# Performance work log

Measured on AMD Instinct MI355X. Metric: run time of the kernel, lower is better.

The kernel has to match this reference:

```python
import jax, jax.numpy as jnp
import numpy as np


def _conv(x, w, pad):
    # NCHW conv, stride 1
    return jax.lax.conv_general_dilated(
        x, w, window_strides=(1, 1), padding=pad,
        dimension_numbers=("NCHW", "OIHW", "NCHW"))


def _deform_conv(x, off_w, off_b, w, b, kh, kw, ph, pw):
    """DCNv2-style modulated deformable conv, stride 1, zero padding."""
    B, C, H, W = x.shape
    K = kh * kw
    om = _conv(x, off_w, ((ph, ph), (pw, pw))) + off_b[None, :, None, None]  # [B,3K,H,W]
    dy, dx, m = om[:, :K], om[:, K:2 * K], om[:, 2 * K:]
    mask = jax.nn.sigmoid(m)  # [B,K,H,W]
    ky = (jnp.repeat(jnp.arange(kh), kw) - ph).astype(x.dtype)  # [K]
    kx = (jnp.tile(jnp.arange(kw), kh) - pw).astype(x.dtype)    # [K]
    hh = jnp.arange(H, dtype=x.dtype)[None, None, :, None]
    ww = jnp.arange(W, dtype=x.dtype)[None, None, None, :]
    py = dy + ky[None, :, None, None] + hh  # [B,K,H,W] sampling y
    px = dx + kx[None, :, None, None] + ww  # [B,K,H,W] sampling x
    y0 = jnp.floor(py)
    x0 = jnp.floor(px)
    ty = py - y0
    tx = px - x0
    y0i = y0.astype(jnp.int32)
    x0i = x0.astype(jnp.int32)
    bidx = jnp.arange(B)[:, None, None, None]

    def gather(yi, xi):
        valid = (yi >= 0) & (yi < H) & (xi >= 0) & (xi < W)
        yc = jnp.clip(yi, 0, H - 1)
        xc = jnp.clip(xi, 0, W - 1)
        v = x[bidx, :, yc, xc]  # [B,K,H,W,C]
        return v * valid[..., None].astype(x.dtype)

    val = (gather(y0i, x0i) * ((1 - ty) * (1 - tx))[..., None]
           + gather(y0i, x0i + 1) * ((1 - ty) * tx)[..., None]
           + gather(y0i + 1, x0i) * (ty * (1 - tx))[..., None]
           + gather(y0i + 1, x0i + 1) * (ty * tx)[..., None])
    val = val * mask[..., None]  # modulation
    out = jnp.einsum('bkhwc,ock->bohw', val, w.reshape(w.shape[0], C, K))
    return out + b[None, :, None, None]


def _preprocess(x, w1, b1, w2, b2):
    h = _conv(x, w1, ((0, 0), (0, 0))) + b1[None, :, None, None]
    return _conv(h, w2, ((0, 0), (0, 0))) + b2[None, :, None, None]


def setup_inputs() -> dict:
    key = jax.random.key(0)
    ks = jax.random.split(key, 12)
    B, C, H, W = 4, 64, 256, 256
    k = 3
    s = 0.05
    inp = {
        "a_low": jax.random.normal(ks[0], (B, C, H, W), jnp.float32),
        "a_high": jax.random.normal(ks[1], (B, C, H, W), jnp.float32),
        # preprocess: Conv 64->32 (1x1), Conv 32->64 (1x1)
        "pre_w1": jax.random.normal(ks[2], (C // 2, C, 1, 1), jnp.float32) * s,
        "pre_b1": jnp.zeros((C // 2,), jnp.float32),
        "pre_w2": jax.random.normal(ks[3], (C, C // 2, 1, 1), jnp.float32) * s,
        "pre_b2": jnp.zeros((C,), jnp.float32),
        # column DCN (3x1 kernel): offset/mask conv -> 3*K channels, K=3
        "offc_w": jax.random.normal(ks[4], (3 * k, C, k, 1), jnp.float32) * 0.01,
        "offc_b": jnp.zeros((3 * k,), jnp.float32),
        "wc": jax.random.normal(ks[5], (C, C, k, 1), jnp.float32) * s,
        "bc": jnp.zeros((C,), jnp.float32),
        # row DCN (1x3 kernel)
        "offr_w": jax.random.normal(ks[6], (3 * k, C, 1, k), jnp.float32) * 0.01,
        "offr_b": jnp.zeros((3 * k,), jnp.float32),
        "wr": jax.random.normal(ks[7], (C, C, 1, k), jnp.float32) * s,
        "br": jnp.zeros((C,), jnp.float32),
    }
    return inp


def reference(a_low, a_high, pre_w1, pre_b1, pre_w2, pre_b2,
              offc_w, offc_b, wc, bc, offr_w, offr_b, wr, br):
    a_low = _preprocess(a_low, pre_w1, pre_b1, pre_w2, pre_b2)
    a_high = _preprocess(a_high, pre_w1, pre_b1, pre_w2, pre_b2)
    # column DCN: kernel (3,1), padding (1,0)
    a_low_c = _deform_conv(a_low, offc_w, offc_b, wc, bc, 3, 1, 1, 0)
    a_colum = a_low + jax.nn.sigmoid(a_low_c) * a_high
    # row DCN: kernel (1,3), padding (0,1)
    a_low_r = _deform_conv(a_low, offr_w, offr_b, wr, br, 1, 3, 0, 1)
    a_row = a_low + jax.nn.sigmoid(a_low_r) * a_high
    return a_row + a_colum
```

## Files before the change

### kernel.cpp

```cpp
#include <hip/hip_runtime.h>
#include <hip/hip_fp16.h>
#include <cmath>

namespace {
constexpr int Bn = 4, Cn = 64, Hn = 256, Wn = 256;
constexpr int HWn = Hn * Wn;
constexpr size_t OFF_PRE_LOW  = 0;
constexpr size_t OFF_PRE_HIGH = 33554432;
constexpr size_t OFF_OM_COL   = 67108864;
constexpr size_t OFF_OM_ROW   = 76546048;
constexpr size_t OFF_WOF16    = 85999616;
constexpr size_t OFF_WPACK    = 86013440;
constexpr size_t OFF_WPRE     = 86062592;
constexpr size_t OFF_BEFF     = 86070784;

constexpr int L_WIN  = 0;
constexpr int L_MOFF = 25920;
constexpr int L_MW   = 27456;
constexpr int L_MG   = 28992;
constexpr int L_MSK  = 32064;
constexpr int L_ZL   = 32832;
constexpr int L_TOT  = 32976;
}

typedef _Float16 f16x8 __attribute__((ext_vector_type(8)));
typedef float f32x4 __attribute__((ext_vector_type(4)));

__device__ __forceinline__ float sigm(float x) { return 1.f / (1.f + __expf(-x)); }
__device__ __forceinline__ __half2 bc2(unsigned u) { return __builtin_bit_cast(__half2, u); }
__device__ __forceinline__ unsigned u32of(__half2 h) { return __builtin_bit_cast(unsigned, h); }

__global__ void k_repack(const float* __restrict__ pw1, const float* __restrict__ pw2,
                         const float* __restrict__ b1,  const float* __restrict__ b2,
                         const float* __restrict__ owc, const float* __restrict__ owr,
                         const float* __restrict__ wc,  const float* __restrict__ wr,
                         char* __restrict__ ws8)
{
    unsigned* Wo2  = (unsigned*)(ws8 + OFF_WOF16);
    __half*   Wp   = (__half*)(ws8 + OFF_WPACK);
    __half*   Wpre = (__half*)(ws8 + OFF_WPRE);
    float*    Beff = (float*)(ws8 + OFF_BEFF);
    int t = blockIdx.x * 256 + threadIdx.x;
    int stride = gridDim.x * 256;
    for (int i = t; i < 3456; i += stride) {
        int ck = i / 18, d = i - ck * 18;
        float v = (d < 9) ? owc[d * 192 + ck] : owr[(d - 9) * 192 + ck];
        Wo2[i] = u32of(__float2half2_rn(v));
    }
    for (int i = t; i < 24576; i += stride) {
        int m = i >= 12288;
        int rem = i - m * 12288;
        int e = rem & 7, l = (rem >> 3) & 63, os = (rem >> 9) & 3, s = rem >> 11;
        int kk = 32 * s + (l >> 4) * 8 + e;
        int o = os * 16 + (l & 15);
        int c = kk & 63, tap = kk >> 6;
        const float* src = m ? wr : wc;
        Wp[i] = __float2half(src[o * 192 + c * 3 + tap]);
    }
    for (int i = t; i < 4096; i += stride) {
        int e = i & 7, l = (i >> 3) & 63, os = (i >> 9) & 3, s = i >> 11;
        int o = os * 16 + (l & 15);
        int c = 32 * s + (l >> 4) * 8 + e;
        float a = 0.f;
        for (int j = 0; j < 32; j++) a += pw2[o * 32 + j] * pw1[j * 64 + c];
        Wpre[i] = __float2half(a);
    }
    for (int i = t; i < 64; i += stride) {
        float a = b2[i];
        for (int j = 0; j < 32; j++) a += pw2[i * 32 + j] * b1[j];
        Beff[i] = a;
    }
}

__global__ __launch_bounds__(256) void k_pre(const float* __restrict__ alow,
                                             const float* __restrict__ ahigh,
                                             char* __restrict__ ws8,
                                             __half* __restrict__ anchw)
{
    __shared__ __align__(16) char XSb[32768];
    int bid = blockIdx.x;
    int tensor = bid >> 10;
    int r = bid & 1023;
    int b = r >> 8, h = r & 255;
    const float* __restrict__ x = (tensor ? ahigh : alow)
                                  + (size_t)b * Cn * HWn + (size_t)h * Wn;
    int tid = threadIdx.x;

#pragma unroll
    for (int it = 0; it < 4; it++) {
        int job = tid + it * 256;
        int c4 = job >> 6, pxg = job & 63;
        int c0 = c4 * 4;
        float4 f0 = *reinterpret_cast<const float4*>(x + (size_t)(c0 + 0) * HWn + pxg * 4);
        float4 f1 = *reinterpret_cast<const float4*>(x + (size_t)(c0 + 1) * HWn + pxg * 4);
        float4 f2 = *reinterpret_cast<const float4*>(x + (size_t)(c0 + 2) * HWn + pxg * 4);
        float4 f3 = *reinterpret_cast<const float4*>(x + (size_t)(c0 + 3) * HWn + pxg * 4);
        const float* p0 = reinterpret_cast<const float*>(&f0);
        const float* p1 = reinterpret_cast<const float*>(&f1);
        const float* p2 = reinterpret_cast<const float*>(&f2);
        const float* p3 = reinterpret_cast<const float*>(&f3);
        int u = c4 >> 1, hf = c4 & 1;
#pragma unroll
        for (int i = 0; i < 4; i++) {
            int px = pxg * 4 + i;
            uint2 v;
            v.x = u32of(__float22half2_rn({p0[i], p1[i]}));
            v.y = u32of(__float22half2_rn({p2[i], p3[i]}));
            *reinterpret_cast<uint2*>(XSb + px * 128 + ((u ^ (px & 7)) * 16) + hf * 8) = v;
        }
    }
    __syncthreads();

    int wv = tid >> 6, lane = tid & 63;
    int kq = lane >> 4, n = lane & 15;
    const f16x8* __restrict__ Wf = (const f16x8*)(ws8 + OFF_WPRE);
    const float* __restrict__ beff = (const float*)(ws8 + OFF_BEFF);
    f16x8 af[8];
#pragma unroll
    for (int i = 0; i < 8; i++) af[i] = Wf[i * 64 + lane];
    f32x4 zero = {0.f, 0.f, 0.f, 0.f};
    f32x4 acc[16];
#pragma unroll
    for (int i = 0; i < 16; i++) acc[i] = zero;
#pragma unroll
    for (int s = 0; s < 2; s++) {
#pragma unroll
        for (int pt = 0; pt < 4; pt++) {
            int px = wv * 64 + pt * 16 + n;
            int u = (4 * s + kq) ^ (px & 7);
            f16x8 bf = *reinterpret_cast<const f16x8*>(XSb + px * 128 + u * 16);
#pragma unroll
            for (int os = 0; os < 4; os++)
                acc[os * 4 + pt] = __builtin_amdgcn_mfma_f32_16x16x32_f16(
                    af[s * 4 + os], bf, acc[os * 4 + pt], 0, 0, 0);
        }
    }
#pragma unroll
    for (int os = 0; os < 4; os++) {
        float4 bq = *reinterpret_cast<const float4*>(beff + os * 16 + kq * 4);
        const float* bqp = reinterpret_cast<const float*>(&bq);
#pragma unroll
        for (int pt = 0; pt < 4; pt++)
#pragma unroll
            for (int rg = 0; rg < 4; rg++) acc[os * 4 + pt][rg] += bqp[rg];
    }

    if (tensor == 0) {
        __half* __restrict__ outp = (__half*)(ws8 + OFF_PRE_LOW) + (size_t)r * 16384;
#pragma unroll
        for (int os = 0; os < 4; os++)
#pragma unroll
            for (int pt = 0; pt < 4; pt++) {
                int px = wv * 64 + pt * 16 + n;
                uint2 v;
                v.x = u32of(__float22half2_rn({acc[os * 4 + pt][0], acc[os * 4 + pt][1]}));
                v.y = u32of(__float22half2_rn({acc[os * 4 + pt][2], acc[os * 4 + pt][3]}));
                *reinterpret_cast<uint2*>(outp + (size_t)px * 64 + os * 16 + kq * 4) = v;
            }
        __half* __restrict__ np = anchw + (size_t)b * Cn * HWn + (size_t)h * Wn;
#pragma unroll
        for (int os = 0; os < 4; os++)
#pragma unroll
            for (int rg = 0; rg < 4; rg++) {
                int o = os * 16 + kq * 4 + rg;
#pragma unroll
                for (int pt = 0; pt < 4; pt++) {
                    int px = wv * 64 + pt * 16 + n;
                    np[(size_t)o * HWn + px] = __float2half(acc[os * 4 + pt][rg]);
                }
            }
    } else {
        __half* __restrict__ np = (__half*)(ws8 + OFF_PRE_HIGH) + (size_t)b * Cn * HWn + (size_t)h * Wn;
#pragma unroll
        for (int os = 0; os < 4; os++)
#pragma unroll
            for (int rg = 0; rg < 4; rg++) {
                int o = os * 16 + kq * 4 + rg;
#pragma unroll
                for (int pt = 0; pt < 4; pt++) {
                    int px = wv * 64 + pt * 16 + n;
                    np[(size_t)o * HWn + px] = __float2half(acc[os * 4 + pt][rg]);
                }
            }
    }
}

__global__ __launch_bounds__(256) void k_om2(const __half* __restrict__ Anc,
                                             const float* __restrict__ ocb,
                                             const float* __restrict__ orb,
                                             char* __restrict__ ws8)
{
    const unsigned* __restrict__ Wo2 = (const unsigned*)(ws8 + OFF_WOF16);
    float* __restrict__ omc = (float*)(ws8 + OFF_OM_COL);
    float* __restrict__ omr = (float*)(ws8 + OFF_OM_ROW);
    int t = blockIdx.x * 256 + threadIdx.x;
    int q = t & 127;
    int h = (t >> 7) & 255;
    int b = t >> 15;
    int w0 = q * 2;
    const __half* __restrict__ base = Anc + ((size_t)b * Cn) * HWn + (size_t)h * Wn + w0;

    const bool topOK = (h > 0), botOK = (h < Hn - 1);
    const bool lOK = (w0 > 0), rOK = (w0 + 2 < Wn);
    const int offT = topOK ? -Wn : 0;
    const int offB = botOK ? Wn : 0;
    const int offL = lOK ? -1 : 0;
    const int offR = rOK ? 2 : 1;

    const __half2 z = __float2half2_rn(0.f);
    const __half hz = __float2half(0.f);
    __half2 aC[9], aR[9];
#pragma unroll
    for (int d = 0; d < 9; d++) { aC[d] = z; aR[d] = z; }

    for (int c = 0; c < 64; c++) {
        const __half* pc = base + (size_t)c * HWn;
        unsigned qm = *reinterpret_cast<const unsigned*>(pc + offT);
        unsigned q0 = *reinterpret_cast<const unsigned*>(pc);
        unsigned qp = *reinterpret_cast<const unsigned*>(pc + offB);
        __half L = lOK ? pc[offL] : hz;
        __half R = rOK ? pc[offR] : hz;
        __half2 m0 = topOK ? bc2(qm) : z;
        __half2 c0 = bc2(q0);
        __half2 p0 = botOK ? bc2(qp) : z;
        __half2 X = __halves2half2(L, __low2half(c0));
        __half2 Z = __halves2half2(__high2half(c0), R);
        const unsigned* wb = Wo2 + c * 54;
#pragma unroll
        for (int d = 0; d < 9; d++) {
            __half2 u0 = bc2(wb[d]), u1 = bc2(wb[18 + d]), u2 = bc2(wb[36 + d]);
            aC[d] = __hfma2(u0, m0, __hfma2(u1, c0, __hfma2(u2, p0, aC[d])));
            __half2 v0 = bc2(wb[9 + d]), v1 = bc2(wb[27 + d]), v2 = bc2(wb[45 + d]);
            aR[d] = __hfma2(v0, X, __hfma2(v1, c0, __hfma2(v2, Z, aR[d])));
        }
    }

    size_t ob = ((size_t)b * 9) * HWn + (size_t)h * Wn + w0;
#pragma unroll
    for (int d = 0; d < 9; d++) {
        float bcd = ocb[d], brd = orb[d];
        float2 vc = { __low2float(aC[d]) + bcd, __high2float(aC[d]) + bcd };
        float2 vr = { __low2float(aR[d]) + brd, __high2float(aR[d]) + brd };
        *reinterpret_cast<float2*>(omc + ob + (size_t)d * HWn) = vc;
        *reinterpret_cast<float2*>(omr + ob + (size_t)d * HWn) = vr;
    }
}

__global__ __launch_bounds__(256, 4) void k_dfuse(const float* __restrict__ bc,
                                                  const float* __restrict__ br,
                                                  float* __restrict__ out,
                                                  char* __restrict__ ws8)
{
    __shared__ __align__(16) char smem8[L_TOT];

    const __half* __restrict__ A16 = (const __half*)(ws8 + OFF_PRE_LOW);

    int bid = blockIdx.x;
    int blk = (bid & 7) * 1024 + (bid >> 3);
    int wt = blk & 7, bh = blk >> 3, h = bh & 255, b = bh >> 8;
    int w0 = wt * 32;
    int tid = threadIdx.x;
    int pbase = b * HWn;

    {
        int ylo = h - 2, xlo = w0 - 2;
#pragma unroll
        for (int i = 0; i < 6; i++) {
            int idx = tid + i * 256;
            if (idx < 1440) {
                int pixw = idx >> 3, ch = idx & 7;
                int r = pixw / 36;
                int xi = pixw - r * 36;
                int y = min(max(ylo + r, 0), Hn - 1);
                int x = min(max(xlo + xi, 0), Wn - 1);
                size_t src = ((size_t)pbase + y * Wn + x) * 64 + ch * 8;
                *reinterpret_cast<uint4*>(smem8 + L_WIN + pixw * 144 + ch * 16) =
                    *reinterpret_cast<const uint4*>(A16 + src);
            }
        }
    }
    if (tid >= 192 && tid < 201) {
        uint4 z4 = {0u, 0u, 0u, 0u};
        *reinterpret_cast<uint4*>(smem8 + L_ZL + (tid - 192) * 16) = z4;
    }

    if (tid < 192) {
        int m = tid >= 96 ? 1 : 0;
        int jj = tid - m * 96;
        int p = jj & 31, tap = jj >> 5;
        int w = w0 + p;
        const float* __restrict__ om = (const float*)(ws8 + (m ? OFF_OM_ROW : OFF_OM_COL));
        size_t ob = ((size_t)b * 9 * Hn + h) * Wn + w;
        float dy = om[ob + (size_t)tap * HWn];
        float dx = om[ob + (size_t)(3 + tap) * HWn];
        float mm = om[ob + (size_t)(6 + tap) * HWn];
        float mask = sigm(mm);
        float py = dy + (float)h + (m ? 0.f : (float)(tap - 1));
        float px = dx + (float)w + (m ? (float)(tap - 1) : 0.f);
        float fy = floorf(py), fx = floorf(px);
        float ty = py - fy, tx = px - fx;
        int y0 = (int)fy, x0 = (int)fx;
        int y1 = y0 + 1, x1 = x0 + 1;
        float vy0 = ((unsigned)y0 < (unsigned)Hn) ? 1.f : 0.f;
        float vy1 = ((unsigned)y1 < (unsigned)Hn) ? 1.f : 0.f;
        float vx0 = ((unsigned)x0 < (unsigned)Wn) ? 1.f : 0.f;
        float vx1 = ((unsigned)x1 < (unsigned)Wn) ? 1.f : 0.f;
        int y0c = min(max(y0, 0), Hn - 1), y1c = min(max(y1, 0), Hn - 1);
        int x0c = min(max(x0, 0), Wn - 1), x1c = min(max(x1, 0), Wn - 1);
        float ry = 1.f - ty, rx = 1.f - tx;
        float w00 = ry * rx * mask * vy0 * vx0;
        float w01 = ry * tx * mask * vy0 * vx1;
        float w10 = ty * rx * mask * vy1 * vx0;
        float w11 = ty * tx * mask * vy1 * vx1;
        int yw0 = y0c - (h - 2), yw1 = y1c - (h - 2);
        int xw0 = x0c - (w0 - 2), xw1 = x1c - (w0 - 2);
        bool i00 = ((unsigned)yw0 < 5u) && ((unsigned)xw0 < 36u);
        bool i01 = ((unsigned)yw0 < 5u) && ((unsigned)xw1 < 36u);
        bool i10 = ((unsigned)yw1 < 5u) && ((unsigned)xw0 < 36u);
        bool i11 = ((unsigned)yw1 < 5u) && ((unsigned)xw1 < 36u);
        ushort4 offs;
        offs.x = i00 ? (ushort)((yw0 * 36 + xw0) * 144) : (ushort)L_ZL;
        offs.y = i01 ? (ushort)((yw0 * 36 + xw1) * 144) : (ushort)L_ZL;
        offs.z = i10 ? (ushort)((yw1 * 36 + xw0) * 144) : (ushort)L_ZL;
        offs.w = i11 ? (ushort)((yw1 * 36 + xw1) * 144) : (ushort)L_ZL;
        *reinterpret_cast<ushort4*>(smem8 + L_MOFF + tid * 8) = offs;
        __half* mw = reinterpret_cast<__half*>(smem8 + L_MW + tid * 8);
        mw[0] = __float2half(w00); mw[1] = __float2half(w01);
        mw[2] = __float2half(w10); mw[3] = __float2half(w11);
        int4 g;
        g.x = (pbase + y0c * Wn + x0c) * 64;
        g.y = (pbase + y0c * Wn + x1c) * 64;
        g.z = (pbase + y1c * Wn + x0c) * 64;
        g.w = (pbase + y1c * Wn + x1c) * 64;
        *reinterpret_cast<int4*>(smem8 + L_MG + tid * 16) = g;
        unsigned msk = (i00 ? 0u : 1u) | (i01 ? 0u : 2u) | (i10 ? 0u : 4u) | (i11 ? 0u : 8u);
        *reinterpret_cast<unsigned*>(smem8 + L_MSK + tid * 4) = msk;
    }
    __syncthreads();

    int wv = tid >> 6, lane = tid & 63;
    int m = wv >> 1, pg = wv & 1;
    int n = lane & 15, kq = lane >> 4;
    int p = pg * 16 + n;
    const f16x8* __restrict__ Wf = (const f16x8*)(ws8 + OFF_WPACK + (size_t)m * 24576);

    f32x4 zero = {0.f, 0.f, 0.f, 0.f};
    f32x4 acc[4] = {zero, zero, zero, zero};
    ushort4 offs = {0, 0, 0, 0};
    __half2 wh0 = {}, wh1 = {}, wh2 = {}, wh3 = {};
    unsigned msk = 0;
    int4 g = {0, 0, 0, 0};
#pragma unroll
    for (int s = 0; s < 6; s++) {
        if ((s & 1) == 0) {
            int idx = m * 96 + (s >> 1) * 32 + p;
            offs = *reinterpret_cast<const ushort4*>(smem8 + L_MOFF + idx * 8);
            uint2 wr_ = *reinterpret_cast<const uint2*>(smem8 + L_MW + idx * 8);
            __half2 wa = bc2(wr_.x), wb = bc2(wr_.y);
            wh0 = __half2half2(__low2half(wa));
            wh1 = __half2half2(__high2half(wa));
            wh2 = __half2half2(__low2half(wb));
            wh3 = __half2half2(__high2half(wb));
            msk = *reinterpret_cast<const unsigned*>(smem8 + L_MSK + idx * 4);
            g = *reinterpret_cast<const int4*>(smem8 + L_MG + idx * 16);
        }
        int co = ((s & 1) << 6) + kq * 16;
        uint4 u0 = *reinterpret_cast<const uint4*>(smem8 + (int)offs.x + co);
        uint4 u1 = *reinterpret_cast<const uint4*>(smem8 + (int)offs.y + co);
        uint4 u2 = *reinterpret_cast<const uint4*>(smem8 + (int)offs.z + co);
        uint4 u3 = *reinterpret_cast<const uint4*>(smem8 + (int)offs.w + co);
        __half2 a0 = __hmul2(bc2(u0.x), wh0);
        __half2 a1 = __hmul2(bc2(u0.y), wh0);
        __half2 a2 = __hmul2(bc2(u0.z), wh0);
        __half2 a3 = __hmul2(bc2(u0.w), wh0);
        a0 = __hfma2(bc2(u1.x), wh1, a0); a1 = __hfma2(bc2(u1.y), wh1, a1);
        a2 = __hfma2(bc2(u1.z), wh1, a2); a3 = __hfma2(bc2(u1.w), wh1, a3);
        a0 = __hfma2(bc2(u2.x), wh2, a0); a1 = __hfma2(bc2(u2.y), wh2, a1);
        a2 = __hfma2(bc2(u2.z), wh2, a2); a3 = __hfma2(bc2(u2.w), wh2, a3);
        a0 = __hfma2(bc2(u3.x), wh3, a0); a1 = __hfma2(bc2(u3.y), wh3, a1);
        a2 = __hfma2(bc2(u3.z), wh3, a2); a3 = __hfma2(bc2(u3.w), wh3, a3);
        if (__any(msk != 0)) {
            int cog = ((s & 1) << 5) + kq * 8;
            if (msk & 1u) { uint4 u = *reinterpret_cast<const uint4*>(A16 + g.x + cog);
                a0 = __hfma2(bc2(u.x), wh0, a0); a1 = __hfma2(bc2(u.y), wh0, a1);
                a2 = __hfma2(bc2(u.z), wh0, a2); a3 = __hfma2(bc2(u.w), wh0, a3); }
            if (msk & 2u) { uint4 u = *reinterpret_cast<const uint4*>(A16 + g.y + cog);
                a0 = __hfma2(bc2(u.x), wh1, a0); a1 = __hfma2(bc2(u.y), wh1, a1);
                a2 = __hfma2(bc2(u.z), wh1, a2); a3 = __hfma2(bc2(u.w), wh1, a3); }
            if (msk & 4u) { uint4 u = *reinterpret_cast<const uint4*>(A16 + g.z + cog);
                a0 = __hfma2(bc2(u.x), wh2, a0); a1 = __hfma2(bc2(u.y), wh2, a1);
                a2 = __hfma2(bc2(u.z), wh2, a2); a3 = __hfma2(bc2(u.w), wh2, a3); }
            if (msk & 8u) { uint4 u = *reinterpret_cast<const uint4*>(A16 + g.w + cog);
                a0 = __hfma2(bc2(u.x), wh3, a0); a1 = __hfma2(bc2(u.y), wh3, a1);
                a2 = __hfma2(bc2(u.z), wh3, a2); a3 = __hfma2(bc2(u.w), wh3, a3); }
        }
        uint4 hb = { u32of(a0), u32of(a1), u32of(a2), u32of(a3) };
        f16x8 bf = __builtin_bit_cast(f16x8, hb);
#pragma unroll
        for (int os = 0; os < 4; os++)
            acc[os] = __builtin_amdgcn_mfma_f32_16x16x32_f16(Wf[(s * 4 + os) * 64 + lane], bf, acc[os], 0, 0, 0);
    }

    const float* __restrict__ bias = m ? br : bc;
    float sg[4][4];
#pragma unroll
    for (int os = 0; os < 4; os++) {
        float4 bq = *reinterpret_cast<const float4*>(bias + os * 16 + kq * 4);
        const float* bqp = reinterpret_cast<const float*>(&bq);
#pragma unroll
        for (int rg = 0; rg < 4; rg++) sg[os][rg] = sigm(acc[os][rg] + bqp[rg]);
    }
    __syncthreads();
    float* EXf = reinterpret_cast<float*>(smem8);
#pragma unroll
    for (int os = 0; os < 4; os++)
#pragma unroll
        for (int rg = 0; rg < 4; rg++)
            EXf[m * 2176 + (os * 16 + kq * 4 + rg) * 34 + p] = sg[os][rg];
    __syncthreads();

    int p2 = tid & 31, og = tid >> 5;
    int o0 = og * 8;
    size_t pix = ((size_t)b * Hn + h) * Wn + (w0 + p2);
    uint4 ua = *reinterpret_cast<const uint4*>(A16 + pix * 64 + o0);
    const __half* ap = reinterpret_cast<const __half*>(&ua);
    const __half* __restrict__ Ahn = (const __half*)(ws8 + OFF_PRE_HIGH);
    size_t chbase = ((size_t)b * 64 + o0) * HWn + (size_t)h * Wn + (w0 + p2);
#pragma unroll
    for (int j = 0; j < 8; j++) {
        float sc = EXf[(o0 + j) * 34 + p2];
        float sr = EXf[2176 + (o0 + j) * 34 + p2];
        float av = __half2float(ap[j]);
        float hv = __half2float(Ahn[chbase + (size_t)j * HWn]);
        out[chbase + (size_t)j * HWn] = 2.f * av + (sc + sr) * hv;
    }
}

extern "C" void kernel_launch(void* const* d_in, const int* in_sizes, int n_in,
                              void* d_out, int out_size, void* d_ws, size_t ws_size,
                              hipStream_t stream)
{
    const float* a_low  = (const float*)d_in[0];
    const float* a_high = (const float*)d_in[1];
    const float* pre_w1 = (const float*)d_in[2];
    const float* pre_b1 = (const float*)d_in[3];
    const float* pre_w2 = (const float*)d_in[4];
    const float* pre_b2 = (const float*)d_in[5];
    const float* offc_w = (const float*)d_in[6];
    const float* offc_b = (const float*)d_in[7];
    const float* wc     = (const float*)d_in[8];
    const float* bc     = (const float*)d_in[9];
    const float* offr_w = (const float*)d_in[10];
    const float* offr_b = (const float*)d_in[11];
    const float* wr     = (const float*)d_in[12];
    const float* br     = (const float*)d_in[13];
    float* out = (float*)d_out;
    char* ws8  = (char*)d_ws;

    hipLaunchKernelGGL(k_repack, dim3(128), dim3(256), 0, stream,
                       pre_w1, pre_w2, pre_b1, pre_b2, offc_w, offr_w, wc, wr, ws8);
    hipLaunchKernelGGL(k_pre, dim3(2048), dim3(256), 0, stream,
                       a_low, a_high, ws8, (__half*)d_out);
    hipLaunchKernelGGL(k_om2, dim3(512), dim3(256), 0, stream,
                       (const __half*)d_out, offc_b, offr_b, ws8);
    hipLaunchKernelGGL(k_dfuse, dim3(8192), dim3(256), 0, stream,
                       bc, br, out, ws8);
}
```

Baseline: 177.0 us.

## Split offset conv across threads and shrink dfuse shared-memory gather metadata

The offset/mask conv kernel now gives the column and row offset convolutions to separate halves of each block. This doubles the grid and halves per-thread accumulators and loads, giving more parallelism and lower register use. In the deformable fuse kernel, per-pixel global gather addresses (int4) are replaced by byte coordinates recomputed on use, and launch bounds go from 4 to 5 blocks per SM to raise occupancy. The cost is more address arithmetic in the rare out-of-window path, and the input rows are now loaded by two thread groups instead of one.

After: 155.2 us. 12.3% less time.

```diff
diff --git a/kernel.cpp b/kernel.cpp
--- a/kernel.cpp
+++ b/kernel.cpp
@@ -17,10 +17,10 @@
 constexpr int L_WIN  = 0;
 constexpr int L_MOFF = 25920;
 constexpr int L_MW   = 27456;
-constexpr int L_MG   = 28992;
-constexpr int L_MSK  = 32064;
-constexpr int L_ZL   = 32832;
-constexpr int L_TOT  = 32976;
+constexpr int L_CRD  = 28992;
+constexpr int L_MSK  = 29760;
+constexpr int L_ZL   = 30528;
+constexpr int L_TOT  = 30672;
 }
 
 typedef _Float16 f16x8 __attribute__((ext_vector_type(8)));
@@ -191,13 +191,11 @@
                                              char* __restrict__ ws8)
 {
     const unsigned* __restrict__ Wo2 = (const unsigned*)(ws8 + OFF_WOF16);
-    float* __restrict__ omc = (float*)(ws8 + OFF_OM_COL);
-    float* __restrict__ omr = (float*)(ws8 + OFF_OM_ROW);
-    int t = blockIdx.x * 256 + threadIdx.x;
-    int q = t & 127;
-    int h = (t >> 7) & 255;
-    int b = t >> 15;
-    int w0 = q * 2;
+    int blk = blockIdx.x;
+    int h = blk & 255, b = blk >> 8;
+    int tid = threadIdx.x;
+    int q2 = tid & 127, md = tid >> 7;
+    int w0 = q2 * 2;
     const __half* __restrict__ base = Anc + ((size_t)b * Cn) * HWn + (size_t)h * Wn + w0;
 
     const bool topOK = (h > 0), botOK = (h < Hn - 1);
@@ -209,44 +207,62 @@
 
     const __half2 z = __float2half2_rn(0.f);
     const __half hz = __float2half(0.f);
-    __half2 aC[9], aR[9];
-#pragma unroll
-    for (int d = 0; d < 9; d++) { aC[d] = z; aR[d] = z; }
-
-    for (int c = 0; c < 64; c++) {
-        const __half* pc = base + (size_t)c * HWn;
-        unsigned qm = *reinterpret_cast<const unsigned*>(pc + offT);
-        unsigned q0 = *reinterpret_cast<const unsigned*>(pc);
-        unsigned qp = *reinterpret_cast<const unsigned*>(pc + offB);
-        __half L = lOK ? pc[offL] : hz;
-        __half R = rOK ? pc[offR] : hz;
-        __half2 m0 = topOK ? bc2(qm) : z;
-        __half2 c0 = bc2(q0);
-        __half2 p0 = botOK ? bc2(qp) : z;
-        __half2 X = __halves2half2(L, __low2half(c0));
-        __half2 Z = __halves2half2(__high2half(c0), R);
-        const unsigned* wb = Wo2 + c * 54;
+    __half2 a[9];
+#pragma unroll
+    for (int d = 0; d < 9; d++) a[d] = z;
+
+    if (md == 0) {
+        for (int c = 0; c < 64; c++) {
+            const __half* pc = base + (size_t)c * HWn;
+            unsigned qm = *reinterpret_cast<const unsigned*>(pc + offT);
+            unsigned q0 = *reinterpret_cast<const unsigned*>(pc);
+            unsigned qp = *reinterpret_cast<const unsigned*>(pc + offB);
+            __half2 m0 = topOK ? bc2(qm) : z;
+            __half2 c0 = bc2(q0);
+            __half2 p0 = botOK ? bc2(qp) : z;
+            const unsigned* wb = Wo2 + c * 54;
+#pragma unroll
+            for (int d = 0; d < 9; d++) {
+                __half2 u0 = bc2(wb[d]), u1 = bc2(wb[18 + d]), u2 = bc2(wb[36 + d]);
+                a[d] = __hfma2(u0, m0, __hfma2(u1, c0, __hfma2(u2, p0, a[d])));
+            }
+        }
+        float* __restrict__ omc = (float*)(ws8 + OFF_OM_COL);
+        size_t ob = ((size_t)b * 9) * HWn + (size_t)h * Wn + w0;
 #pragma unroll
         for (int d = 0; d < 9; d++) {
-            __half2 u0 = bc2(wb[d]), u1 = bc2(wb[18 + d]), u2 = bc2(wb[36 + d]);
-            aC[d] = __hfma2(u0, m0, __hfma2(u1, c0, __hfma2(u2, p0, aC[d])));
-            __half2 v0 = bc2(wb[9 + d]), v1 = bc2(wb[27 + d]), v2 = bc2(wb[45 + d]);
-            aR[d] = __hfma2(v0, X, __hfma2(v1, c0, __hfma2(v2, Z, aR[d])));
-        }
-    }
-
-    size_t ob = ((size_t)b * 9) * HWn + (size_t)h * Wn + w0;
-#pragma unroll
-    for (int d = 0; d < 9; d++) {
-        float bcd = ocb[d], brd = orb[d];
-        float2 vc = { __low2float(aC[d]) + bcd, __high2float(aC[d]) + bcd };
-        float2 vr = { __low2float(aR[d]) + brd, __high2float(aR[d]) + brd };
-        *reinterpret_cast<float2*>(omc + ob + (size_t)d * HWn) = vc;
-        *reinterpret_cast<float2*>(omr + ob + (size_t)d * HWn) = vr;
-    }
-}
-
-__global__ __launch_bounds__(256, 4) void k_dfuse(const float* __restrict__ bc,
+            float bcd = ocb[d];
+            float2 vc = { __low2float(a[d]) + bcd, __high2float(a[d]) + bcd };
+            *reinterpret_cast<float2*>(omc + ob + (size_t)d * HWn) = vc;
+        }
+    } else {
+        for (int c = 0; c < 64; c++) {
+            const __half* pc = base + (size_t)c * HWn;
+            unsigned q0 = *reinterpret_cast<const unsigned*>(pc);
+            __half L = lOK ? pc[offL] : hz;
+            __half R = rOK ? pc[offR] : hz;
+            __half2 c0 = bc2(q0);
+            __half2 X = __halves2half2(L, __low2half(c0));
+            __half2 Z = __halves2half2(__high2half(c0), R);
+            const unsigned* wb = Wo2 + c * 54;
+#pragma unroll
+            for (int d = 0; d < 9; d++) {
+                __half2 v0 = bc2(wb[9 + d]), v1 = bc2(wb[27 + d]), v2 = bc2(wb[45 + d]);
+                a[d] = __hfma2(v0, X, __hfma2(v1, c0, __hfma2(v2, Z, a[d])));
+            }
+        }
+        float* __restrict__ omr = (float*)(ws8 + OFF_OM_ROW);
+        size_t ob = ((size_t)b * 9) * HWn + (size_t)h * Wn + w0;
+#pragma unroll
+        for (int d = 0; d < 9; d++) {
+            float brd = orb[d];
+            float2 vr = { __low2float(a[d]) + brd, __high2float(a[d]) + brd };
+            *reinterpret_cast<float2*>(omr + ob + (size_t)d * HWn) = vr;
+        }
+    }
+}
+
+__global__ __launch_bounds__(256, 5) void k_dfuse(const float* __restrict__ bc,
                                                   const float* __restrict__ br,
                                                   float* __restrict__ out,
                                                   char* __restrict__ ws8)
@@ -327,12 +343,9 @@
         __half* mw = reinterpret_cast<__half*>(smem8 + L_MW + tid * 8);
         mw[0] = __float2half(w00); mw[1] = __float2half(w01);
         mw[2] = __float2half(w10); mw[3] = __float2half(w11);
-        int4 g;
-        g.x = (pbase + y0c * Wn + x0c) * 64;
-        g.y = (pbase + y0c * Wn + x1c) * 64;
-        g.z = (pbase + y1c * Wn + x0c) * 64;
-        g.w = (pbase + y1c * Wn + x1c) * 64;
-        *reinterpret_cast<int4*>(smem8 + L_MG + tid * 16) = g;
+        uchar4 cr = { (unsigned char)y0c, (unsigned char)x0c,
+                      (unsigned char)y1c, (unsigned char)x1c };
+        *reinterpret_cast<uchar4*>(smem8 + L_CRD + tid * 4) = cr;
         unsigned msk = (i00 ? 0u : 1u) | (i01 ? 0u : 2u) | (i10 ? 0u : 4u) | (i11 ? 0u : 8u);
         *reinterpret_cast<unsigned*>(smem8 + L_MSK + tid * 4) = msk;
     }
@@ -349,7 +362,7 @@
     ushort4 offs = {0, 0, 0, 0};
     __half2 wh0 = {}, wh1 = {}, wh2 = {}, wh3 = {};
     unsigned msk = 0;
-    int4 g = {0, 0, 0, 0};
+    uchar4 cr = {0, 0, 0, 0};
 #pragma unroll
     for (int s = 0; s < 6; s++) {
         if ((s & 1) == 0) {
@@ -362,7 +375,7 @@
             wh2 = __half2half2(__low2half(wb));
             wh3 = __half2half2(__high2half(wb));
             msk = *reinterpret_cast<const unsigned*>(smem8 + L_MSK + idx * 4);
-            g = *reinterpret_cast<const int4*>(smem8 + L_MG + idx * 16);
+            cr = *reinterpret_cast<const uchar4*>(smem8 + L_CRD + idx * 4);
         }
         int co = ((s & 1) << 6) + kq * 16;
         uint4 u0 = *reinterpret_cast<const uint4*>(smem8 + (int)offs.x + co);
@@ -381,16 +394,24 @@
         a2 = __hfma2(bc2(u3.z), wh3, a2); a3 = __hfma2(bc2(u3.w), wh3, a3);
         if (__any(msk != 0)) {
             int cog = ((s & 1) << 5) + kq * 8;
-            if (msk & 1u) { uint4 u = *reinterpret_cast<const uint4*>(A16 + g.x + cog);
+            if (msk & 1u) {
+                int gx = (pbase + (int)cr.x * Wn + (int)cr.y) * 64;
+                uint4 u = *reinterpret_cast<const uint4*>(A16 + gx + cog);
                 a0 = __hfma2(bc2(u.x), wh0, a0); a1 = __hfma2(bc2(u.y), wh0, a1);
                 a2 = __hfma2(bc2(u.z), wh0, a2); a3 = __hfma2(bc2(u.w), wh0, a3); }
-            if (msk & 2u) { uint4 u = *reinterpret_cast<const uint4*>(A16 + g.y + cog);
+            if (msk & 2u) {
+                int gx = (pbase + (int)cr.x * Wn + (int)cr.w) * 64;
+                uint4 u = *reinterpret_cast<const uint4*>(A16 + gx + cog);
                 a0 = __hfma2(bc2(u.x), wh1, a0); a1 = __hfma2(bc2(u.y), wh1, a1);
                 a2 = __hfma2(bc2(u.z), wh1, a2); a3 = __hfma2(bc2(u.w), wh1, a3); }
-            if (msk & 4u) { uint4 u = *reinterpret_cast<const uint4*>(A16 + g.z + cog);
+            if (msk & 4u) {
+                int gx = (pbase + (int)cr.z * Wn + (int)cr.y) * 64;
+                uint4 u = *reinterpret_cast<const uint4*>(A16 + gx + cog);
                 a0 = __hfma2(bc2(u.x), wh2, a0); a1 = __hfma2(bc2(u.y), wh2, a1);
                 a2 = __hfma2(bc2(u.z), wh2, a2); a3 = __hfma2(bc2(u.w), wh2, a3); }
-            if (msk & 8u) { uint4 u = *reinterpret_cast<const uint4*>(A16 + g.w + cog);
+            if (msk & 8u) {
+                int gx = (pbase + (int)cr.z * Wn + (int)cr.w) * 64;
+                uint4 u = *reinterpret_cast<const uint4*>(A16 + gx + cog);
                 a0 = __hfma2(bc2(u.x), wh3, a0); a1 = __hfma2(bc2(u.y), wh3, a1);
                 a2 = __hfma2(bc2(u.z), wh3, a2); a3 = __hfma2(bc2(u.w), wh3, a3); }
         }
@@ -461,7 +482,7 @@
                        pre_w1, pre_w2, pre_b1, pre_b2, offc_w, offr_w, wc, wr, ws8);
     hipLaunchKernelGGL(k_pre, dim3(2048), dim3(256), 0, stream,
                        a_low, a_high, ws8, (__half*)d_out);
-    hipLaunchKernelGGL(k_om2, dim3(512), dim3(256), 0, stream,
+    hipLaunchKernelGGL(k_om2, dim3(1024), dim3(256), 0, stream,
                        (const __half*)d_out, offc_b, offr_b, ws8);
     hipLaunchKernelGGL(k_dfuse, dim3(8192), dim3(256), 0, stream,
                        bc, br, out, ws8);
```
